# Performance work log

Measured on AMD Instinct MI355X. Metric: run time of the kernel, lower is better.

The kernel has to match this reference:

```python
import jax, jax.numpy as jnp
import numpy as np

B, T, F, H, M = 128, 64, 2048, 1024, 512


def setup_inputs() -> dict:
    key = jax.random.key(0)
    ks = jax.random.split(key, 12)
    def u(k, shape, fan_in):
        s = 1.0 / np.sqrt(fan_in)
        return jax.random.uniform(k, shape, jnp.float32, -s, s)
    return {
        "video_feats": jax.random.normal(ks[0], (B, T, F), jnp.float32),
        # frame_embed: Linear(F -> H)
        "W_embed": u(ks[1], (H, F), F),
        "b_embed": u(ks[2], (H,), F),
        # lstm1_cell: LSTMCell(H, H) with bias (b = b_ih + b_hh, identical math)
        "W_ih1": u(ks[3], (4 * H, H), H),
        "W_hh1": u(ks[4], (4 * H, H), H),
        "b1": u(ks[5], (4 * H,), H),
        # BoundaryDetector(H, H, M): z = sigmoid(vs . (Wsi x + Wsh h + b)), binarized
        "Wsi": u(ks[6], (M, H), H),
        "Wsh": u(ks[7], (M, H), H),
        "b_bd": u(ks[8], (M,), H),
        "vs": u(ks[9], (M,), M),
        # lstm2_cell: LSTMCell(H, H, bias=False)
        "W_ih2": u(ks[10], (4 * H, H), H),
        "W_hh2": u(ks[11], (4 * H, H), H),
    }


def _lstm_cell(x, h, c, W_ih, W_hh, b):
    # PyTorch LSTMCell gate order: i, f, g, o
    gates = x @ W_ih.T + h @ W_hh.T
    if b is not None:
        gates = gates + b
    i, f, g, o = jnp.split(gates, 4, axis=-1)
    c_new = jax.nn.sigmoid(f) * c + jax.nn.sigmoid(i) * jnp.tanh(g)
    h_new = jax.nn.sigmoid(o) * jnp.tanh(c_new)
    return h_new, c_new


def reference(video_feats, W_embed, b_embed, W_ih1, W_hh1, b1,
              Wsi, Wsh, b_bd, vs, W_ih2, W_hh2):
    # frame embedding + ReLU (dropout is identity in eval mode)
    v = jax.nn.relu(jnp.einsum('btf,hf->bth', video_feats, W_embed) + b_embed)
    vt = jnp.transpose(v, (1, 0, 2))  # [T, B, H] for scan over time

    def step(carry, x):
        h1, c1, h2, c2 = carry
        # boundary detector: scalar gate per sample, straight-through binarized
        z = jax.nn.sigmoid((x @ Wsi.T + h1 @ Wsh.T + b_bd) @ vs)  # [B]
        s = (z + jax.lax.stop_gradient(jnp.round(z) - z))[:, None]  # [B,1]
        h1n, c1n = _lstm_cell(x, h1, c1, W_ih1, W_hh1, b1)
        h2n, c2n = _lstm_cell(h1n * s, h2, c2, W_ih2, W_hh2, None)
        h1n = h1n * (1.0 - s)
        c1n = c1n * (1.0 - s)
        return (h1n, c1n, h2n, c2n), None

    z0 = jnp.zeros((B, H), video_feats.dtype)
    (h1, c1, h2, c2), _ = jax.lax.scan(step, (z0, z0, z0, z0), vt)
    return h2
```

## Files before the change

kernel.cpp:

```cpp
#include <hip/hip_runtime.h>
#include <hip/hip_bf16.h>
#include <math.h>


typedef __attribute__((ext_vector_type(8))) short short8;
typedef __attribute__((ext_vector_type(4))) short short4v;
typedef __attribute__((ext_vector_type(4))) float f32x4;
typedef __hip_bfloat16 bf16;

__device__ __forceinline__ float sigm(float x) { return 1.0f / (1.0f + expf(-x)); }
__device__ __forceinline__ short bfbits(float x) {
  bf16 h = __float2bfloat16(x);
  return __builtin_bit_cast(short, h);
}
__device__ __forceinline__ void cvtfp(const f32x4 a, const f32x4 b,
                                      short8& hi, short8& lo)
{
#pragma unroll
  for (int j = 0; j < 8; ++j) {
    float x = (j < 4) ? a[j] : b[j - 4];
    bf16 h = __float2bfloat16(x);
    hi[j] = __builtin_bit_cast(short, h);
    lo[j] = bfbits(x - __bfloat162float(h));
  }
}

#define TILE 8192
#define BUF  32768

#define STAGE_IDX                                              \
  int srow[4], sseg[4], ssw[4];                                \
  _Pragma("unroll")                                            \
  for (int i = 0; i < 4; ++i) {                                \
    int linear = i * 256 + threadIdx.x;                        \
    srow[i] = linear >> 3;                                     \
    sseg[i] = linear & 7;                                      \
    ssw[i]  = (sseg[i] ^ (srow[i] & 7)) * 8;                   \
  }

#define FRAG_IDX                                               \
  const int lane = threadIdx.x & 63, wave = threadIdx.x >> 6;  \
  const int wr = (wave & 1) * 64, wc = (wave >> 1) * 64;       \
  const int m = lane & 15, kg = lane >> 4;

__device__ __forceinline__ void gemm3(
    const bf16* __restrict__ Ah, const bf16* __restrict__ Al,
    const bf16* __restrict__ Bh, const bf16* __restrict__ Bl,
    int nChunks, const float* __restrict__ smk, int pol,
    short* ls, f32x4 acc[4][4])
{
  STAGE_IDX
  FRAG_IDX
  bool keep[4];
#pragma unroll
  for (int i = 0; i < 4; ++i)
    keep[i] = (smk == nullptr) || ((smk[srow[i]] > 0.5f) == (pol != 0));

  const short8 zz = {};
  short8 rah[4], ral[4], rbh[4], rbl[4];

  auto LOAD = [&](int c) {
#pragma unroll
    for (int i = 0; i < 4; ++i) {
      size_t o = (size_t)srow[i] * 1024 + c * 64 + sseg[i] * 8;
      rah[i] = keep[i] ? *(const short8*)(Ah + o) : zz;
      ral[i] = keep[i] ? *(const short8*)(Al + o) : zz;
      rbh[i] = *(const short8*)(Bh + o);
      rbl[i] = *(const short8*)(Bl + o);
    }
  };
  auto STORE = [&](int buf) {
    short* p = ls + buf * BUF;
#pragma unroll
    for (int i = 0; i < 4; ++i) {
      int o = srow[i] * 64 + ssw[i];
      *(short8*)(p + o)            = rah[i];
      *(short8*)(p + TILE + o)     = ral[i];
      *(short8*)(p + 2 * TILE + o) = rbh[i];
      *(short8*)(p + 3 * TILE + o) = rbl[i];
    }
  };

  LOAD(0); STORE(0);
  if (nChunks > 1) LOAD(1);
  __syncthreads();

  for (int c = 0; c < nChunks; ++c) {
    if (c + 1 < nChunks) STORE((c + 1) & 1);
    if (c + 2 < nChunks) LOAD(c + 2);
    const short* la = ls + (c & 1) * BUF;
#pragma unroll
    for (int ks = 0; ks < 2; ++ks) {
      short8 afh[4], afl[4], bfh[4], bfl[4];
      int asw[4], bsw[4];
#pragma unroll
      for (int f = 0; f < 4; ++f) {
        int ar = wr + f * 16 + m;
        asw[f] = ar * 64 + (((ks * 4 + kg) ^ (ar & 7)) * 8);
        int br = wc + f * 16 + m;
        bsw[f] = br * 64 + (((ks * 4 + kg) ^ (br & 7)) * 8);
        afh[f] = *(const short8*)(la + asw[f]);
        bfh[f] = *(const short8*)(la + 2 * TILE + bsw[f]);
      }
#pragma unroll
      for (int fr = 0; fr < 4; ++fr)
#pragma unroll
        for (int fc = 0; fc < 4; ++fc)
          acc[fr][fc] = __builtin_amdgcn_mfma_f32_16x16x32_bf16(afh[fr], bfh[fc], acc[fr][fc], 0, 0, 0);
#pragma unroll
      for (int f = 0; f < 4; ++f)
        afl[f] = *(const short8*)(la + TILE + asw[f]);
#pragma unroll
      for (int fr = 0; fr < 4; ++fr)
#pragma unroll
        for (int fc = 0; fc < 4; ++fc)
          acc[fr][fc] = __builtin_amdgcn_mfma_f32_16x16x32_bf16(afl[fr], bfh[fc], acc[fr][fc], 0, 0, 0);
#pragma unroll
      for (int f = 0; f < 4; ++f)
        bfl[f] = *(const short8*)(la + 3 * TILE + bsw[f]);
#pragma unroll
      for (int fr = 0; fr < 4; ++fr)
#pragma unroll
        for (int fc = 0; fc < 4; ++fc)
          acc[fr][fc] = __builtin_amdgcn_mfma_f32_16x16x32_bf16(afh[fr], bfl[fc], acc[fr][fc], 0, 0, 0);
    }
    if (c + 1 < nChunks) __syncthreads();
  }
}

__device__ __forceinline__ void gemm2(
    const bf16* __restrict__ Ah, const bf16* __restrict__ Al,
    const bf16* __restrict__ B,
    int nChunks, const float* __restrict__ smk, int pol,
    short* ls, f32x4 acc[4][4])
{
  STAGE_IDX
  FRAG_IDX
  bool keep[4];
#pragma unroll
  for (int i = 0; i < 4; ++i)
    keep[i] = (smk == nullptr) || ((smk[srow[i]] > 0.5f) == (pol != 0));

  const short8 zz = {};
  short8 rah[4], ral[4], rb[4];

  auto LOAD = [&](int c) {
#pragma unroll
    for (int i = 0; i < 4; ++i) {
      size_t o = (size_t)srow[i] * 1024 + c * 64 + sseg[i] * 8;
      rah[i] = keep[i] ? *(const short8*)(Ah + o) : zz;
      ral[i] = keep[i] ? *(const short8*)(Al + o) : zz;
      rb[i]  = *(const short8*)(B + o);
    }
  };
  auto STORE = [&](int buf) {
    short* p = ls + buf * BUF;
#pragma unroll
    for (int i = 0; i < 4; ++i) {
      int o = srow[i] * 64 + ssw[i];
      *(short8*)(p + o)            = rah[i];
      *(short8*)(p + TILE + o)     = ral[i];
      *(short8*)(p + 2 * TILE + o) = rb[i];
    }
  };

  LOAD(0); STORE(0);
  if (nChunks > 1) LOAD(1);
  __syncthreads();

  for (int c = 0; c < nChunks; ++c) {
    if (c + 1 < nChunks) STORE((c + 1) & 1);
    if (c + 2 < nChunks) LOAD(c + 2);
    const short* la = ls + (c & 1) * BUF;
#pragma unroll
    for (int ks = 0; ks < 2; ++ks) {
      short8 afh[4], afl[4], bf[4];
      int asw[4], bsw[4];
#pragma unroll
      for (int f = 0; f < 4; ++f) {
        int ar = wr + f * 16 + m;
        asw[f] = ar * 64 + (((ks * 4 + kg) ^ (ar & 7)) * 8);
        int br = wc + f * 16 + m;
        bsw[f] = br * 64 + (((ks * 4 + kg) ^ (br & 7)) * 8);
        afh[f] = *(const short8*)(la + asw[f]);
        bf[f]  = *(const short8*)(la + 2 * TILE + bsw[f]);
      }
#pragma unroll
      for (int fr = 0; fr < 4; ++fr)
#pragma unroll
        for (int fc = 0; fc < 4; ++fc)
          acc[fr][fc] = __builtin_amdgcn_mfma_f32_16x16x32_bf16(afh[fr], bf[fc], acc[fr][fc], 0, 0, 0);
#pragma unroll
      for (int f = 0; f < 4; ++f)
        afl[f] = *(const short8*)(la + TILE + asw[f]);
#pragma unroll
      for (int fr = 0; fr < 4; ++fr)
#pragma unroll
        for (int fc = 0; fc < 4; ++fc)
          acc[fr][fc] = __builtin_amdgcn_mfma_f32_16x16x32_bf16(afl[fr], bf[fc], acc[fr][fc], 0, 0, 0);
    }
    if (c + 1 < nChunks) __syncthreads();
  }
}

template <typename F>
__device__ __forceinline__ void epilogue(const f32x4 acc[4][4], F&& body)
{
  FRAG_IDX
#pragma unroll
  for (int fr = 0; fr < 4; ++fr)
#pragma unroll
    for (int fc = 0; fc < 4; ++fc)
#pragma unroll
      for (int r = 0; r < 4; ++r)
        body(wr + fr * 16 + kg * 4 + r, wc + fc * 16 + m, acc[fr][fc][r]);
}

__global__ void k_diag(float* __restrict__ out, float val)
{
  if (threadIdx.x == 0 && blockIdx.x == 0) out[0] = val;
}

__global__ void k_uw(const float* __restrict__ Wsi, const float* __restrict__ Wsh,
                     const float* __restrict__ bbd, const float* __restrict__ vs,
                     double* __restrict__ u, double* __restrict__ wv,
                     double* __restrict__ cbdp)
{
  const int blk = blockIdx.x;
  if (blk < 8) {
    const float* W = (blk < 4) ? Wsi : Wsh;
    double* out = (blk < 4) ? u : wv;
    int h = (blk & 3) * 256 + threadIdx.x;
    double a = 0.0;
    for (int mm = 0; mm < 512; ++mm)
      a += (double)vs[mm] * (double)W[mm * 1024 + h];
    out[h] = a;
  } else if (threadIdx.x < 64) {
    double a = 0.0;
    for (int mm = threadIdx.x; mm < 512; mm += 64)
      a += (double)vs[mm] * (double)bbd[mm];
#pragma unroll
    for (int o = 32; o > 0; o >>= 1) a += __shfl_down(a, o, 64);
    if (threadIdx.x == 0) cbdp[0] = a;
  }
}

__global__ void k_wsplit(const float* __restrict__ w1hh, const float* __restrict__ w2ih,
                         const float* __restrict__ w2hh,
                         bf16* __restrict__ o1hh_h, bf16* __restrict__ o1hh_l,
                         bf16* __restrict__ o2ih_h, bf16* __restrict__ o2hh_h)
{
  const int m = blockIdx.x >> 12;
  const size_t i4 = (size_t)(blockIdx.x & 4095) * 256 + threadIdx.x;
  const float* src = (m == 0) ? w1hh : (m == 1) ? w2ih : w2hh;
  bf16* dh = (m == 0) ? o1hh_h : (m == 1) ? o2ih_h : o2hh_h;
  bf16* dl = (m == 0) ? o1hh_l : nullptr;
  f32x4 v = *(const f32x4*)(src + i4 * 4);
  short4v hv, lv;
#pragma unroll
  for (int j = 0; j < 4; ++j) {
    float x = v[j];
    bf16 h = __float2bfloat16(x);
    hv[j] = __builtin_bit_cast(short, h);
    lv[j] = bfbits(x - __bfloat162float(h));
  }
  *(short4v*)((short*)dh + i4 * 4) = hv;
  if (dl) *(short4v*)((short*)dl + i4 * 4) = lv;
}

__global__ __launch_bounds__(256, 1) void k_embed(
    const float* __restrict__ video, const float* __restrict__ Wemb,
    float* __restrict__ Ep, int tbase)
{
  __shared__ __align__(16) short ls[65536];
  const int tl = blockIdx.x >> 5;
  const int ct = (blockIdx.x >> 2) & 7;
  const int kh = blockIdx.x & 3;

  STAGE_IDX
  FRAG_IDX
  const float* arow[4];
  const float* brow[4];
#pragma unroll
  for (int i = 0; i < 4; ++i) {
    arow[i] = video + (size_t)(srow[i] * 64 + tbase + tl) * 2048 + kh * 512 + sseg[i] * 8;
    brow[i] = Wemb + (size_t)(ct * 128 + srow[i]) * 2048 + kh * 512 + sseg[i] * 8;
  }

  f32x4 fa[4][2], fb[4][2];
  auto LOAD = [&](int c) {
#pragma unroll
    for (int i = 0; i < 4; ++i) {
      fa[i][0] = *(const f32x4*)(arow[i] + c * 64);
      fa[i][1] = *(const f32x4*)(arow[i] + c * 64 + 4);
      fb[i][0] = *(const f32x4*)(brow[i] + c * 64);
      fb[i][1] = *(const f32x4*)(brow[i] + c * 64 + 4);
    }
  };
  auto STORE = [&](int buf) {
    short* p = ls + buf * BUF;
#pragma unroll
    for (int i = 0; i < 4; ++i) {
      short8 hi, lo;
      int o = srow[i] * 64 + ssw[i];
      cvtfp(fa[i][0], fa[i][1], hi, lo);
      *(short8*)(p + o)        = hi;
      *(short8*)(p + TILE + o) = lo;
      cvtfp(fb[i][0], fb[i][1], hi, lo);
      *(short8*)(p + 2 * TILE + o) = hi;
      *(short8*)(p + 3 * TILE + o) = lo;
    }
  };

  f32x4 acc[4][4] = {};
  LOAD(0); STORE(0);
  LOAD(1);
  __syncthreads();

  for (int c = 0; c < 8; ++c) {
    if (c + 1 < 8) STORE((c + 1) & 1);
    if (c + 2 < 8) LOAD(c + 2);
    const short* la = ls + (c & 1) * BUF;
#pragma unroll
    for (int ks = 0; ks < 2; ++ks) {
      short8 afh[4], afl[4], bfh[4], bfl[4];
      int asw[4], bsw[4];
#pragma unroll
      for (int f = 0; f < 4; ++f) {
        int ar = wr + f * 16 + m;
        asw[f] = ar * 64 + (((ks * 4 + kg) ^ (ar & 7)) * 8);
        int br = wc + f * 16 + m;
        bsw[f] = br * 64 + (((ks * 4 + kg) ^ (br & 7)) * 8);
        afh[f] = *(const short8*)(la + asw[f]);
        bfh[f] = *(const short8*)(la + 2 * TILE + bsw[f]);
      }
#pragma unroll
      for (int fr = 0; fr < 4; ++fr)
#pragma unroll
        for (int fc = 0; fc < 4; ++fc)
          acc[fr][fc] = __builtin_amdgcn_mfma_f32_16x16x32_bf16(afh[fr], bfh[fc], acc[fr][fc], 0, 0, 0);
#pragma unroll
      for (int f = 0; f < 4; ++f)
        afl[f] = *(const short8*)(la + TILE + asw[f]);
#pragma unroll
      for (int fr = 0; fr < 4; ++fr)
#pragma unroll
        for (int fc = 0; fc < 4; ++fc)
          acc[fr][fc] = __builtin_amdgcn_mfma_f32_16x16x32_bf16(afl[fr], bfh[fc], acc[fr][fc], 0, 0, 0);
#pragma unroll
      for (int f = 0; f < 4; ++f)
        bfl[f] = *(const short8*)(la + 3 * TILE + bsw[f]);
#pragma unroll
      for (int fr = 0; fr < 4; ++fr)
#pragma unroll
        for (int fc = 0; fc < 4; ++fc)
          acc[fr][fc] = __builtin_amdgcn_mfma_f32_16x16x32_bf16(afh[fr], bfl[fc], acc[fr][fc], 0, 0, 0);
    }
    if (c + 1 < 8) __syncthreads();
  }

  epilogue(acc, [&](int lrow, int lcol, float aval) {
    Ep[(size_t)kh * 1048576 + (size_t)(tl * 128 + lrow) * 1024 + ct * 128 + lcol] = aval;
  });
}

__global__ void k_efin(const float* __restrict__ Ep, const float* __restrict__ bemb,
                       bf16* __restrict__ vhi, bf16* __restrict__ vlo)
{
  const size_t e = ((size_t)blockIdx.x * 256 + threadIdx.x) * 4;
  f32x4 a0 = *(const f32x4*)(Ep + e);
  f32x4 a1 = *(const f32x4*)(Ep + 1048576 + e);
  f32x4 a2 = *(const f32x4*)(Ep + 2097152 + e);
  f32x4 a3 = *(const f32x4*)(Ep + 3145728 + e);
  f32x4 bb = *(const f32x4*)(bemb + (e & 1023));
  short4v hv, lv;
#pragma unroll
  for (int j = 0; j < 4; ++j) {
    float x = a0[j] + a1[j] + a2[j] + a3[j] + bb[j];
    x = fmaxf(x, 0.0f);
    bf16 h = __float2bfloat16(x);
    hv[j] = __builtin_bit_cast(short, h);
    lv[j] = bfbits(x - __bfloat162float(h));
  }
  *(short4v*)((short*)vhi + e) = hv;
  *(short4v*)((short*)vlo + e) = lv;
}

__global__ __launch_bounds__(256, 1) void k_xgates(
    const bf16* __restrict__ vhi, const bf16* __restrict__ vlo,
    const float* __restrict__ Wih1, float* __restrict__ Gx)
{
  __shared__ __align__(16) short ls[65536];
  const int x  = blockIdx.x & 7;
  const int s  = blockIdx.x >> 3;
  const int ct = x * 4 + (s & 3);
  const int rt = s >> 2;

  STAGE_IDX
  FRAG_IDX
  const bf16* arh[4];
  const bf16* arl[4];
  const float* brow[4];
#pragma unroll
  for (int i = 0; i < 4; ++i) {
    arh[i] = vhi + (size_t)rt * 131072 + (size_t)srow[i] * 1024 + sseg[i] * 8;
    arl[i] = vlo + (size_t)rt * 131072 + (size_t)srow[i] * 1024 + sseg[i] * 8;
    brow[i] = Wih1 + (size_t)(ct * 128 + srow[i]) * 1024 + sseg[i] * 8;
  }

  short8 rah[4], ral[4];
  f32x4 fb[4][2];
  auto LOAD = [&](int c) {
#pragma unroll
    for (int i = 0; i < 4; ++i) {
      rah[i] = *(const short8*)(arh[i] + c * 64);
      ral[i] = *(const short8*)(arl[i] + c * 64);
      fb[i][0] = *(const f32x4*)(brow[i] + c * 64);
      fb[i][1] = *(const f32x4*)(brow[i] + c * 64 + 4);
    }
  };
  auto STORE = [&](int buf) {
    short* p = ls + buf * BUF;
#pragma unroll
    for (int i = 0; i < 4; ++i) {
      int o = srow[i] * 64 + ssw[i];
      *(short8*)(p + o)        = rah[i];
      *(short8*)(p + TILE + o) = ral[i];
      short8 hi, lo;
      cvtfp(fb[i][0], fb[i][1], hi, lo);
      *(short8*)(p + 2 * TILE + o) = hi;
      *(short8*)(p + 3 * TILE + o) = lo;
    }
  };

  f32x4 acc[4][4] = {};
  LOAD(0); STORE(0);
  LOAD(1);
  __syncthreads();

  for (int c = 0; c < 16; ++c) {
    if (c + 1 < 16) STORE((c + 1) & 1);
    if (c + 2 < 16) LOAD(c + 2);
    const short* la = ls + (c & 1) * BUF;
#pragma unroll
    for (int ks = 0; ks < 2; ++ks) {
      short8 afh[4], afl[4], bfh[4], bfl[4];
      int asw[4], bsw[4];
#pragma unroll
      for (int f = 0; f < 4; ++f) {
        int ar = wr + f * 16 + m;
        asw[f] = ar * 64 + (((ks * 4 + kg) ^ (ar & 7)) * 8);
        int br = wc + f * 16 + m;
        bsw[f] = br * 64 + (((ks * 4 + kg) ^ (br & 7)) * 8);
        afh[f] = *(const short8*)(la + asw[f]);
        bfh[f] = *(const short8*)(la + 2 * TILE + bsw[f]);
      }
#pragma unroll
      for (int fr = 0; fr < 4; ++fr)
#pragma unroll
        for (int fc = 0; fc < 4; ++fc)
          acc[fr][fc] = __builtin_amdgcn_mfma_f32_16x16x32_bf16(afh[fr], bfh[fc], acc[fr][fc], 0, 0, 0);
#pragma unroll
      for (int f = 0; f < 4; ++f)
        afl[f] = *(const short8*)(la + TILE + asw[f]);
#pragma unroll
      for (int fr = 0; fr < 4; ++fr)
#pragma unroll
        for (int fc = 0; fc < 4; ++fc)
          acc[fr][fc] = __builtin_amdgcn_mfma_f32_16x16x32_bf16(afl[fr], bfh[fc], acc[fr][fc], 0, 0, 0);
#pragma unroll
      for (int f = 0; f < 4; ++f)
        bfl[f] = *(const short8*)(la + 3 * TILE + bsw[f]);
#pragma unroll
      for (int fr = 0; fr < 4; ++fr)
#pragma unroll
        for (int fc = 0; fc < 4; ++fc)
          acc[fr][fc] = __builtin_amdgcn_mfma_f32_16x16x32_bf16(afh[fr], bfl[fc], acc[fr][fc], 0, 0, 0);
    }
    if (c + 1 < 16) __syncthreads();
  }

  epilogue(acc, [&](int lrow, int lcol, float aval) {
    Gx[(size_t)rt * 524288 + (size_t)lrow * 4096 + ct * 128 + lcol] = aval;
  });
}

__global__ __launch_bounds__(256, 1) void k_step(
    const bf16* __restrict__ h1nh, const bf16* __restrict__ h1nl,
    const bf16* __restrict__ h2h, const bf16* __restrict__ h2l,
    const bf16* __restrict__ w1hh_h, const bf16* __restrict__ w1hh_l,
    const bf16* __restrict__ w2ih_h, const bf16* __restrict__ w2hh_h,
    const float* __restrict__ sm, float* __restrict__ R, int k)
{
  __shared__ __align__(16) short ls[65536];
  const int job = blockIdx.x >> 5;
  const int ct  = blockIdx.x & 31;
  if (k == 64 && job < 4) return;

  f32x4 acc[4][4] = {};
  const size_t cto = (size_t)ct * 131072;
  if (job < 4) {
    const size_t ko = (size_t)job * 256;
    gemm3(h1nh + ko, h1nl + ko, w1hh_h + cto + ko, w1hh_l + cto + ko,
          4, sm, 0, ls, acc);
  } else if (job < 6) {
    const size_t ko = (size_t)(job - 4) * 512;
    gemm2(h1nh + ko, h1nl + ko, w2ih_h + cto + ko, 8, sm, 1, ls, acc);
  } else {
    const size_t ko = (size_t)(job - 6) * 512;
    gemm2(h2h + ko, h2l + ko, w2hh_h + cto + ko, 8, nullptr, 0, ls, acc);
  }

  float* Rout = R + (size_t)(job >> 1) * 524288;
  epilogue(acc, [&](int lrow, int lcol, float aval) {
    atomicAdd(&Rout[(size_t)lrow * 4096 + ct * 128 + lcol], aval);
  });
}

__global__ void k_elem(float* __restrict__ R, const float* __restrict__ Gx,
                       const bf16* __restrict__ vhi, const bf16* __restrict__ vlo,
                       const double* __restrict__ uvec, const double* __restrict__ cbdp,
                       float* __restrict__ craw,
                       bf16* __restrict__ h1nh, bf16* __restrict__ h1nl,
                       float* __restrict__ sm,
                       float* __restrict__ c2, bf16* __restrict__ h2h, bf16* __restrict__ h2l,
                       float* __restrict__ rdm, const double* __restrict__ wv,
                       const float* __restrict__ b1, float* __restrict__ dout, int k)
{
  __shared__ double red[8];
  const int tid = threadIdx.x;
  const int b   = blockIdx.x;
  const size_t broff = (size_t)b * 4096;
  float* P0 = R + broff;
  float* P1 = P0 + 524288;
  float* P2 = P0 + 2 * 524288;
  float* P3 = P0 + 3 * 524288;
  const float* GX = Gx + (size_t)(k & 7) * 524288 + broff;

  if (k < 64) {
    const bf16* vhr = vhi + (size_t)(k & 7) * 131072 + (size_t)b * 1024;
    const bf16* vlr = vlo + (size_t)(k & 7) * 131072 + (size_t)b * 1024;
    double za = 0.0;
#pragma unroll
    for (int ji = 0; ji < 2; ++ji) {
      int j = tid + ji * 512;
      za += (double)(__bfloat162float(vhr[j]) + __bfloat162float(vlr[j])) * uvec[j];
    }
#pragma unroll
    for (int o = 32; o > 0; o >>= 1) za += __shfl_down(za, o, 64);
    if ((tid & 63) == 0) red[tid >> 6] = za;
    __syncthreads();
    float zpre = (float)(red[0] + red[1] + red[2] + red[3] +
                         red[4] + red[5] + red[6] + red[7] + cbdp[0]);
    if (k > 0) zpre += rdm[(k - 1) * 128 + b];
    float s  = (sigm(zpre) > 0.5f) ? 1.0f : 0.0f;
    float om = 1.0f - s;
    __syncthreads();

    double rd = 0.0;
#pragma unroll
    for (int ji = 0; ji < 2; ++ji) {
      int j = tid + ji * 512;
      float gi = GX[j]        + b1[j];
      float gf = GX[1024 + j] + b1[1024 + j];
      float gg = GX[2048 + j] + b1[2048 + j];
      float go = GX[3072 + j] + b1[3072 + j];
      if (k > 0) {
        gi += P0[j]        + P1[j];
        gf += P0[1024 + j] + P1[1024 + j];
        gg += P0[2048 + j] + P1[2048 + j];
        go += P0[3072 + j] + P1[3072 + j];
        P0[j] = 0.0f; P0[1024 + j] = 0.0f; P0[2048 + j] = 0.0f; P0[3072 + j] = 0.0f;
        P1[j] = 0.0f; P1[1024 + j] = 0.0f; P1[2048 + j] = 0.0f; P1[3072 + j] = 0.0f;
      }
      float cn = sigm(gf) * craw[b * 1024 + j] + sigm(gi) * tanhf(gg);
      float hn = sigm(go) * tanhf(cn);
      craw[b * 1024 + j] = om * cn;
      bf16 hh = __float2bfloat16(hn);
      h1nh[b * 1024 + j] = hh;
      h1nl[b * 1024 + j] = __float2bfloat16(hn - __bfloat162float(hh));
      rd += (double)hn * wv[j];
    }
#pragma unroll
    for (int o = 32; o > 0; o >>= 1) rd += __shfl_down(rd, o, 64);
    if ((tid & 63) == 0) red[tid >> 6] = rd;
    __syncthreads();
    if (tid == 0) {
      rdm[k * 128 + b] = om * (float)(red[0] + red[1] + red[2] + red[3] +
                                      red[4] + red[5] + red[6] + red[7]);
      sm[b] = s;
    }
  }

  if (k >= 1) {
#pragma unroll
    for (int ji = 0; ji < 2; ++ji) {
      int j = tid + ji * 512;
      float gi = P2[j]        + P3[j];
      float gf = P2[1024 + j] + P3[1024 + j];
      float gg = P2[2048 + j] + P3[2048 + j];
      float go = P2[3072 + j] + P3[3072 + j];
      P2[j] = 0.0f; P2[1024 + j] = 0.0f; P2[2048 + j] = 0.0f; P2[3072 + j] = 0.0f;
      P3[j] = 0.0f; P3[1024 + j] = 0.0f; P3[2048 + j] = 0.0f; P3[3072 + j] = 0.0f;
      float cn = sigm(gf) * c2[b * 1024 + j] + sigm(gi) * tanhf(gg);
      float hn = sigm(go) * tanhf(cn);
      c2[b * 1024 + j] = cn;
      bf16 hh = __float2bfloat16(hn);
      h2h[b * 1024 + j] = hh;
      h2l[b * 1024 + j] = __float2bfloat16(hn - __bfloat162float(hh));
      if (k == 64) dout[b * 1024 + j] = hn;
    }
  }
}

extern "C" void kernel_launch(void* const* d_in, const int* in_sizes, int n_in,
                              void* d_out, int out_size, void* d_ws, size_t ws_size,
                              hipStream_t stream) {
  const float* video = (const float*)d_in[0];
  const float* Wemb  = (const float*)d_in[1];
  const float* bemb  = (const float*)d_in[2];
  const float* Wih1  = (const float*)d_in[3];
  const float* Whh1  = (const float*)d_in[4];
  const float* b1    = (const float*)d_in[5];
  const float* Wsi   = (const float*)d_in[6];
  const float* Wsh   = (const float*)d_in[7];
  const float* bbd   = (const float*)d_in[8];
  const float* vs    = (const float*)d_in[9];
  const float* Wih2  = (const float*)d_in[10];
  const float* Whh2  = (const float*)d_in[11];
  float* dout = (float*)d_out;

  static const int exp_sizes[12] = {
    128 * 64 * 2048, 1024 * 2048, 1024, 4096 * 1024, 4096 * 1024, 4096,
    512 * 1024, 512 * 1024, 512, 512, 4096 * 1024, 4096 * 1024 };
  int bad = -1;
  if (n_in != 12) bad = 99;
  else if (out_size != 131072) bad = 98;
  else
    for (int i = 0; i < 12; ++i)
      if (in_sizes[i] != exp_sizes[i]) { bad = i; break; }
  if (bad >= 0) {
    k_diag<<<1, 64, 0, stream>>>(dout, 10000.0f + (float)bad);
    return;
  }

  char* ws = (char*)d_ws;
  size_t off = 0;
  auto alloc = [&](size_t bytes) {
    char* p = ws + off;
    off += (bytes + 255) & ~(size_t)255;
    return p;
  };
  bf16*  h1nh = (bf16*)alloc(262144);
  bf16*  h1nl = (bf16*)alloc(262144);
  bf16*  h2h  = (bf16*)alloc(262144);
  bf16*  h2l  = (bf16*)alloc(262144);
  float* c2   = (float*)alloc(524288);
  float* craw = (float*)alloc(524288);
  float* sm   = (float*)alloc(512);
  const size_t zeroBytes = off;
  double* u    = (double*)alloc(8192);
  double* wvv  = (double*)alloc(8192);
  double* cbdp = (double*)alloc(256);
  float* rdm   = (float*)alloc(64 * 128 * 4);
  bf16* w1hh_h = (bf16*)alloc(8388608);
  bf16* w1hh_l = (bf16*)alloc(8388608);
  bf16* w2ih_h = (bf16*)alloc(8388608);
  bf16* w2hh_h = (bf16*)alloc(8388608);
  float* R     = (float*)alloc(4 * 2097152);
  float* Gxf   = (float*)alloc(8 * 2097152);
  bf16* vhi    = (bf16*)alloc(8 * 131072 * 2);
  bf16* vlo    = (bf16*)alloc(8 * 131072 * 2);

  if (ws_size < off) {
    k_diag<<<1, 64, 0, stream>>>(dout, 100.0f + (float)(ws_size >> 20));
    return;
  }

  (void)hipMemsetAsync(d_ws, 0, zeroBytes, stream);
  (void)hipMemsetAsync(R, 0, 4 * 2097152, stream);
  k_uw<<<9, 256, 0, stream>>>(Wsi, Wsh, bbd, vs, u, wvv, cbdp);
  k_wsplit<<<12288, 256, 0, stream>>>(Whh1, Wih2, Whh2,
                                      w1hh_h, w1hh_l, w2ih_h, w2hh_h);

  for (int k = 0; k <= 64; ++k) {
    if (k < 64 && (k & 7) == 0) {
      k_embed<<<256, 256, 0, stream>>>(video, Wemb, Gxf, k);
      k_efin<<<1024, 256, 0, stream>>>(Gxf, bemb, vhi, vlo);
      k_xgates<<<256, 256, 0, stream>>>(vhi, vlo, Wih1, Gxf);
    }
    if (k > 0)
      k_step<<<256, 256, 0, stream>>>(h1nh, h1nl, h2h, h2l,
                                      w1hh_h, w1hh_l, w2ih_h, w2hh_h, sm, R, k);
    k_elem<<<128, 512, 0, stream>>>(R, Gxf, vhi, vlo, u, cbdp, craw,
                                    h1nh, h1nl, sm, c2, h2h, h2l,
                                    rdm, wvv, b1, dout, k);
  }
}
```

Before: 2.632 ms.

## Split GEMM K dimension across more blocks with single-buffered LDS and atomics

```diff
diff --git a/kernel.cpp b/kernel.cpp
--- a/kernel.cpp
+++ b/kernel.cpp
@@ -69,26 +69,22 @@
       rbl[i] = *(const short8*)(Bl + o);
     }
   };
-  auto STORE = [&](int buf) {
-    short* p = ls + buf * BUF;
+  auto STORE = [&]() {
 #pragma unroll
     for (int i = 0; i < 4; ++i) {
       int o = srow[i] * 64 + ssw[i];
-      *(short8*)(p + o)            = rah[i];
-      *(short8*)(p + TILE + o)     = ral[i];
-      *(short8*)(p + 2 * TILE + o) = rbh[i];
-      *(short8*)(p + 3 * TILE + o) = rbl[i];
-    }
-  };
-
-  LOAD(0); STORE(0);
+      *(short8*)(ls + o)            = rah[i];
+      *(short8*)(ls + TILE + o)     = ral[i];
+      *(short8*)(ls + 2 * TILE + o) = rbh[i];
+      *(short8*)(ls + 3 * TILE + o) = rbl[i];
+    }
+  };
+
+  LOAD(0); STORE();
   if (nChunks > 1) LOAD(1);
   __syncthreads();
 
   for (int c = 0; c < nChunks; ++c) {
-    if (c + 1 < nChunks) STORE((c + 1) & 1);
-    if (c + 2 < nChunks) LOAD(c + 2);
-    const short* la = ls + (c & 1) * BUF;
 #pragma unroll
     for (int ks = 0; ks < 2; ++ks) {
       short8 afh[4], afl[4], bfh[4], bfl[4];
@@ -99,8 +95,8 @@
         asw[f] = ar * 64 + (((ks * 4 + kg) ^ (ar & 7)) * 8);
         int br = wc + f * 16 + m;
         bsw[f] = br * 64 + (((ks * 4 + kg) ^ (br & 7)) * 8);
-        afh[f] = *(const short8*)(la + asw[f]);
-        bfh[f] = *(const short8*)(la + 2 * TILE + bsw[f]);
+        afh[f] = *(const short8*)(ls + asw[f]);
+        bfh[f] = *(const short8*)(ls + 2 * TILE + bsw[f]);
       }
 #pragma unroll
       for (int fr = 0; fr < 4; ++fr)
@@ -109,7 +105,7 @@
           acc[fr][fc] = __builtin_amdgcn_mfma_f32_16x16x32_bf16(afh[fr], bfh[fc], acc[fr][fc], 0, 0, 0);
 #pragma unroll
       for (int f = 0; f < 4; ++f)
-        afl[f] = *(const short8*)(la + TILE + asw[f]);
+        afl[f] = *(const short8*)(ls + TILE + asw[f]);
 #pragma unroll
       for (int fr = 0; fr < 4; ++fr)
 #pragma unroll
@@ -117,14 +113,19 @@
           acc[fr][fc] = __builtin_amdgcn_mfma_f32_16x16x32_bf16(afl[fr], bfh[fc], acc[fr][fc], 0, 0, 0);
 #pragma unroll
       for (int f = 0; f < 4; ++f)
-        bfl[f] = *(const short8*)(la + 3 * TILE + bsw[f]);
+        bfl[f] = *(const short8*)(ls + 3 * TILE + bsw[f]);
 #pragma unroll
       for (int fr = 0; fr < 4; ++fr)
 #pragma unroll
         for (int fc = 0; fc < 4; ++fc)
           acc[fr][fc] = __builtin_amdgcn_mfma_f32_16x16x32_bf16(afh[fr], bfl[fc], acc[fr][fc], 0, 0, 0);
     }
-    if (c + 1 < nChunks) __syncthreads();
+    if (c + 1 < nChunks) {
+      __syncthreads();
+      STORE();
+      if (c + 2 < nChunks) LOAD(c + 2);
+      __syncthreads();
+    }
   }
 }
 
@@ -153,25 +154,21 @@
       rb[i]  = *(const short8*)(B + o);
     }
   };
-  auto STORE = [&](int buf) {
-    short* p = ls + buf * BUF;
+  auto STORE = [&]() {
 #pragma unroll
     for (int i = 0; i < 4; ++i) {
       int o = srow[i] * 64 + ssw[i];
-      *(short8*)(p + o)            = rah[i];
-      *(short8*)(p + TILE + o)     = ral[i];
-      *(short8*)(p + 2 * TILE + o) = rb[i];
-    }
-  };
-
-  LOAD(0); STORE(0);
+      *(short8*)(ls + o)            = rah[i];
+      *(short8*)(ls + TILE + o)     = ral[i];
+      *(short8*)(ls + 2 * TILE + o) = rb[i];
+    }
+  };
+
+  LOAD(0); STORE();
   if (nChunks > 1) LOAD(1);
   __syncthreads();
 
   for (int c = 0; c < nChunks; ++c) {
-    if (c + 1 < nChunks) STORE((c + 1) & 1);
-    if (c + 2 < nChunks) LOAD(c + 2);
-    const short* la = ls + (c & 1) * BUF;
 #pragma unroll
     for (int ks = 0; ks < 2; ++ks) {
       short8 afh[4], afl[4], bf[4];
@@ -182,8 +179,8 @@
         asw[f] = ar * 64 + (((ks * 4 + kg) ^ (ar & 7)) * 8);
         int br = wc + f * 16 + m;
         bsw[f] = br * 64 + (((ks * 4 + kg) ^ (br & 7)) * 8);
-        afh[f] = *(const short8*)(la + asw[f]);
-        bf[f]  = *(const short8*)(la + 2 * TILE + bsw[f]);
+        afh[f] = *(const short8*)(ls + asw[f]);
+        bf[f]  = *(const short8*)(ls + 2 * TILE + bsw[f]);
       }
 #pragma unroll
       for (int fr = 0; fr < 4; ++fr)
@@ -192,14 +189,19 @@
           acc[fr][fc] = __builtin_amdgcn_mfma_f32_16x16x32_bf16(afh[fr], bf[fc], acc[fr][fc], 0, 0, 0);
 #pragma unroll
       for (int f = 0; f < 4; ++f)
-        afl[f] = *(const short8*)(la + TILE + asw[f]);
+        afl[f] = *(const short8*)(ls + TILE + asw[f]);
 #pragma unroll
       for (int fr = 0; fr < 4; ++fr)
 #pragma unroll
         for (int fc = 0; fc < 4; ++fc)
           acc[fr][fc] = __builtin_amdgcn_mfma_f32_16x16x32_bf16(afl[fr], bf[fc], acc[fr][fc], 0, 0, 0);
     }
-    if (c + 1 < nChunks) __syncthreads();
+    if (c + 1 < nChunks) {
+      __syncthreads();
+      STORE();
+      if (c + 2 < nChunks) LOAD(c + 2);
+      __syncthreads();
+    }
   }
 }
 
@@ -226,22 +228,33 @@
                      double* __restrict__ u, double* __restrict__ wv,
                      double* __restrict__ cbdp)
 {
+  __shared__ double red[256];
   const int blk = blockIdx.x;
-  if (blk < 8) {
-    const float* W = (blk < 4) ? Wsi : Wsh;
-    double* out = (blk < 4) ? u : wv;
-    int h = (blk & 3) * 256 + threadIdx.x;
+  const int tid = threadIdx.x;
+  if (blk < 64) {
+    const float* W = (blk < 32) ? Wsi : Wsh;
+    double* out = (blk < 32) ? u : wv;
+    const int hbase = (blk & 31) * 32;
+    const int h = hbase + (tid & 31);
+    const int g = tid >> 5;
     double a = 0.0;
-    for (int mm = 0; mm < 512; ++mm)
+    for (int mm = g * 64; mm < g * 64 + 64; ++mm)
       a += (double)vs[mm] * (double)W[mm * 1024 + h];
-    out[h] = a;
-  } else if (threadIdx.x < 64) {
+    red[tid] = a;
+    __syncthreads();
+    if (tid < 32) {
+      double sum = 0.0;
+#pragma unroll
+      for (int g2 = 0; g2 < 8; ++g2) sum += red[g2 * 32 + tid];
+      out[hbase + tid] = sum;
+    }
+  } else if (tid < 64) {
     double a = 0.0;
-    for (int mm = threadIdx.x; mm < 512; mm += 64)
+    for (int mm = tid; mm < 512; mm += 64)
       a += (double)vs[mm] * (double)bbd[mm];
 #pragma unroll
     for (int o = 32; o > 0; o >>= 1) a += __shfl_down(a, o, 64);
-    if (threadIdx.x == 0) cbdp[0] = a;
+    if (tid == 0) cbdp[0] = a;
   }
 }
 
@@ -386,15 +399,16 @@
   *(short4v*)((short*)vlo + e) = lv;
 }
 
-__global__ __launch_bounds__(256, 1) void k_xgates(
+__global__ __launch_bounds__(256, 2) void k_xgates(
     const bf16* __restrict__ vhi, const bf16* __restrict__ vlo,
     const float* __restrict__ Wih1, float* __restrict__ Gx)
 {
-  __shared__ __align__(16) short ls[65536];
+  __shared__ __align__(16) short ls[32768];
   const int x  = blockIdx.x & 7;
   const int s  = blockIdx.x >> 3;
   const int ct = x * 4 + (s & 3);
-  const int rt = s >> 2;
+  const int rt = (s >> 2) & 7;
+  const int kh = s >> 5;
 
   STAGE_IDX
   FRAG_IDX
@@ -403,9 +417,10 @@
   const float* brow[4];
 #pragma unroll
   for (int i = 0; i < 4; ++i) {
-    arh[i] = vhi + (size_t)rt * 131072 + (size_t)srow[i] * 1024 + sseg[i] * 8;
-    arl[i] = vlo + (size_t)rt * 131072 + (size_t)srow[i] * 1024 + sseg[i] * 8;
-    brow[i] = Wih1 + (size_t)(ct * 128 + srow[i]) * 1024 + sseg[i] * 8;
+    size_t ro = (size_t)srow[i] * 1024 + kh * 512 + sseg[i] * 8;
+    arh[i] = vhi + (size_t)rt * 131072 + ro;
+    arl[i] = vlo + (size_t)rt * 131072 + ro;
+    brow[i] = Wih1 + (size_t)(ct * 128 + srow[i]) * 1024 + kh * 512 + sseg[i] * 8;
   }
 
   short8 rah[4], ral[4];
@@ -419,29 +434,25 @@
       fb[i][1] = *(const f32x4*)(brow[i] + c * 64 + 4);
     }
   };
-  auto STORE = [&](int buf) {
-    short* p = ls + buf * BUF;
+  auto STORE = [&]() {
 #pragma unroll
     for (int i = 0; i < 4; ++i) {
       int o = srow[i] * 64 + ssw[i];
-      *(short8*)(p + o)        = rah[i];
-      *(short8*)(p + TILE + o) = ral[i];
+      *(short8*)(ls + o)        = rah[i];
+      *(short8*)(ls + TILE + o) = ral[i];
       short8 hi, lo;
       cvtfp(fb[i][0], fb[i][1], hi, lo);
-      *(short8*)(p + 2 * TILE + o) = hi;
-      *(short8*)(p + 3 * TILE + o) = lo;
+      *(short8*)(ls + 2 * TILE + o) = hi;
+      *(short8*)(ls + 3 * TILE + o) = lo;
     }
   };
 
   f32x4 acc[4][4] = {};
-  LOAD(0); STORE(0);
+  LOAD(0); STORE();
   LOAD(1);
   __syncthreads();
 
-  for (int c = 0; c < 16; ++c) {
-    if (c + 1 < 16) STORE((c + 1) & 1);
-    if (c + 2 < 16) LOAD(c + 2);
-    const short* la = ls + (c & 1) * BUF;
+  for (int c = 0; c < 8; ++c) {
 #pragma unroll
     for (int ks = 0; ks < 2; ++ks) {
       short8 afh[4], afl[4], bfh[4], bfl[4];
@@ -452,8 +463,8 @@
         asw[f] = ar * 64 + (((ks * 4 + kg) ^ (ar & 7)) * 8);
         int br = wc + f * 16 + m;
         bsw[f] = br * 64 + (((ks * 4 + kg) ^ (br & 7)) * 8);
-        afh[f] = *(const short8*)(la + asw[f]);
-        bfh[f] = *(const short8*)(la + 2 * TILE + bsw[f]);
+        afh[f] = *(const short8*)(ls + asw[f]);
+        bfh[f] = *(const short8*)(ls + 2 * TILE + bsw[f]);
       }
 #pragma unroll
       for (int fr = 0; fr < 4; ++fr)
@@ -462,7 +473,7 @@
           acc[fr][fc] = __builtin_amdgcn_mfma_f32_16x16x32_bf16(afh[fr], bfh[fc], acc[fr][fc], 0, 0, 0);
 #pragma unroll
       for (int f = 0; f < 4; ++f)
-        afl[f] = *(const short8*)(la + TILE + asw[f]);
+        afl[f] = *(const short8*)(ls + TILE + asw[f]);
 #pragma unroll
       for (int fr = 0; fr < 4; ++fr)
 #pragma unroll
@@ -470,48 +481,57 @@
           acc[fr][fc] = __builtin_amdgcn_mfma_f32_16x16x32_bf16(afl[fr], bfh[fc], acc[fr][fc], 0, 0, 0);
 #pragma unroll
       for (int f = 0; f < 4; ++f)
-        bfl[f] = *(const short8*)(la + 3 * TILE + bsw[f]);
+        bfl[f] = *(const short8*)(ls + 3 * TILE + bsw[f]);
 #pragma unroll
       for (int fr = 0; fr < 4; ++fr)
 #pragma unroll
         for (int fc = 0; fc < 4; ++fc)
           acc[fr][fc] = __builtin_amdgcn_mfma_f32_16x16x32_bf16(afh[fr], bfl[fc], acc[fr][fc], 0, 0, 0);
     }
-    if (c + 1 < 16) __syncthreads();
+    if (c + 1 < 8) {
+      __syncthreads();
+      STORE();
+      if (c + 2 < 8) LOAD(c + 2);
+      __syncthreads();
+    }
   }
 
   epilogue(acc, [&](int lrow, int lcol, float aval) {
-    Gx[(size_t)rt * 524288 + (size_t)lrow * 4096 + ct * 128 + lcol] = aval;
+    atomicAdd(&Gx[(size_t)rt * 524288 + (size_t)lrow * 4096 + ct * 128 + lcol], aval);
   });
 }
 
-__global__ __launch_bounds__(256, 1) void k_step(
+__global__ __launch_bounds__(256, 2) void k_step(
     const bf16* __restrict__ h1nh, const bf16* __restrict__ h1nl,
     const bf16* __restrict__ h2h, const bf16* __restrict__ h2l,
     const bf16* __restrict__ w1hh_h, const bf16* __restrict__ w1hh_l,
     const bf16* __restrict__ w2ih_h, const bf16* __restrict__ w2hh_h,
     const float* __restrict__ sm, float* __restrict__ R, int k)
 {
-  __shared__ __align__(16) short ls[65536];
+  __shared__ __align__(16) short ls[32768];
   const int job = blockIdx.x >> 5;
   const int ct  = blockIdx.x & 31;
-  if (k == 64 && job < 4) return;
+  if (k == 64 && job < 8) return;
 
   f32x4 acc[4][4] = {};
   const size_t cto = (size_t)ct * 131072;
-  if (job < 4) {
-    const size_t ko = (size_t)job * 256;
+  int idx;
+  if (job < 8) {
+    const size_t ko = (size_t)job * 128;
     gemm3(h1nh + ko, h1nl + ko, w1hh_h + cto + ko, w1hh_l + cto + ko,
-          4, sm, 0, ls, acc);
-  } else if (job < 6) {
-    const size_t ko = (size_t)(job - 4) * 512;
-    gemm2(h1nh + ko, h1nl + ko, w2ih_h + cto + ko, 8, sm, 1, ls, acc);
+          2, sm, 0, ls, acc);
+    idx = 0;
+  } else if (job < 12) {
+    const size_t ko = (size_t)(job - 8) * 256;
+    gemm2(h1nh + ko, h1nl + ko, w2ih_h + cto + ko, 4, sm, 1, ls, acc);
+    idx = 2;
   } else {
-    const size_t ko = (size_t)(job - 6) * 512;
-    gemm2(h2h + ko, h2l + ko, w2hh_h + cto + ko, 8, nullptr, 0, ls, acc);
-  }
-
-  float* Rout = R + (size_t)(job >> 1) * 524288;
+    const size_t ko = (size_t)(job - 12) * 256;
+    gemm2(h2h + ko, h2l + ko, w2hh_h + cto + ko, 4, nullptr, 0, ls, acc);
+    idx = 3;
+  }
+
+  float* Rout = R + (size_t)idx * 524288;
   epilogue(acc, [&](int lrow, int lcol, float aval) {
     atomicAdd(&Rout[(size_t)lrow * 4096 + ct * 128 + lcol], aval);
   });
@@ -532,7 +552,6 @@
   const int b   = blockIdx.x;
   const size_t broff = (size_t)b * 4096;
   float* P0 = R + broff;
-  float* P1 = P0 + 524288;
   float* P2 = P0 + 2 * 524288;
   float* P3 = P0 + 3 * 524288;
   const float* GX = Gx + (size_t)(k & 7) * 524288 + broff;
@@ -566,12 +585,11 @@
       float gg = GX[2048 + j] + b1[2048 + j];
       float go = GX[3072 + j] + b1[3072 + j];
       if (k > 0) {
-        gi += P0[j]        + P1[j];
-        gf += P0[1024 + j] + P1[1024 + j];
-        gg += P0[2048 + j] + P1[2048 + j];
-        go += P0[3072 + j] + P1[3072 + j];
+        gi += P0[j];
+        gf += P0[1024 + j];
+        gg += P0[2048 + j];
+        go += P0[3072 + j];
         P0[j] = 0.0f; P0[1024 + j] = 0.0f; P0[2048 + j] = 0.0f; P0[3072 + j] = 0.0f;
-        P1[j] = 0.0f; P1[1024 + j] = 0.0f; P1[2048 + j] = 0.0f; P1[3072 + j] = 0.0f;
       }
       float cn = sigm(gf) * craw[b * 1024 + j] + sigm(gi) * tanhf(gg);
       float hn = sigm(go) * tanhf(cn);
@@ -679,7 +697,7 @@
 
   (void)hipMemsetAsync(d_ws, 0, zeroBytes, stream);
   (void)hipMemsetAsync(R, 0, 4 * 2097152, stream);
-  k_uw<<<9, 256, 0, stream>>>(Wsi, Wsh, bbd, vs, u, wvv, cbdp);
+  k_uw<<<65, 256, 0, stream>>>(Wsi, Wsh, bbd, vs, u, wvv, cbdp);
   k_wsplit<<<12288, 256, 0, stream>>>(Whh1, Wih2, Whh2,
                                       w1hh_h, w1hh_l, w2ih_h, w2hh_h);
 
@@ -687,10 +705,11 @@
     if (k < 64 && (k & 7) == 0) {
       k_embed<<<256, 256, 0, stream>>>(video, Wemb, Gxf, k);
       k_efin<<<1024, 256, 0, stream>>>(Gxf, bemb, vhi, vlo);
-      k_xgates<<<256, 256, 0, stream>>>(vhi, vlo, Wih1, Gxf);
+      (void)hipMemsetAsync(Gxf, 0, 8 * 2097152, stream);
+      k_xgates<<<512, 256, 0, stream>>>(vhi, vlo, Wih1, Gxf);
     }
     if (k > 0)
-      k_step<<<256, 256, 0, stream>>>(h1nh, h1nl, h2h, h2l,
+      k_step<<<512, 256, 0, stream>>>(h1nh, h1nl, h2h, h2l,
                                       w1hh_h, w1hh_l, w2ih_h, w2hh_h, sm, R, k);
     k_elem<<<128, 512, 0, stream>>>(R, Gxf, vhi, vlo, u, cbdp, craw,
                                     h1nh, h1nl, sm, c2, h2h, h2l,
```

Measured after the change: 3.375 ms. 1.28x slower.
